# Optimization experiments

Measured on AMD Instinct MI355X. Metric: run time of the kernel, lower is better.

## Reference

```python
import jax, jax.numpy as jnp
import numpy as np
import math

EPS = 1e-5

def layernorm(x, w):
    mu = jnp.mean(x, axis=-1, keepdims=True)
    var = jnp.var(x, axis=-1, keepdims=True)
    return (x - mu) * jax.lax.rsqrt(var + EPS) * w

def setup_inputs() -> dict:
    key = jax.random.key(0)
    ks = jax.random.split(key, 6)
    B, T, C = 2, 2048, 768
    s = 0.02
    return {
        "x": jax.random.normal(ks[0], (B, T, C), jnp.float32),
        "w_ln1": jnp.ones((C,), jnp.float32),
        "w_attn": jax.random.normal(ks[1], (C, 3 * C), jnp.float32) * s,
        "w_attn_proj": jax.random.normal(ks[2], (C, C), jnp.float32) * s,
        "w_ln2": jnp.ones((C,), jnp.float32),
        "w_fc": jax.random.normal(ks[3], (C, 4 * C), jnp.float32) * s,
        "w_mlp_proj": jax.random.normal(ks[4], (4 * C, C), jnp.float32) * s,
    }

def _attention(x, w_attn, w_attn_proj, n_head):
    B, T, C = x.shape
    D = C // n_head
    qkv = x @ w_attn  # [B,T,3C]
    q, k, v = jnp.split(qkv, 3, axis=-1)
    # [B,H,T,D]
    q = q.reshape(B, T, n_head, D).transpose(0, 2, 1, 3)
    k = k.reshape(B, T, n_head, D).transpose(0, 2, 1, 3)
    v = v.reshape(B, T, n_head, D).transpose(0, 2, 1, 3)
    # squared L2 distance via ||q||^2 + ||k||^2 - 2 q.k (same math, no [B,H,T,T,D] tensor)
    q2 = jnp.sum(q * q, axis=-1)  # [B,H,T]
    k2 = jnp.sum(k * k, axis=-1)  # [B,H,T]
    qk = jnp.einsum('bhqd,bhkd->bhqk', q, k)
    sq_l2 = q2[..., :, None] + k2[..., None, :] - 2.0 * qk  # [B,H,T,T]
    scale = -1.0 / (2.0 * math.sqrt(D))
    scores = jnp.exp(sq_l2 * scale)
    causal = jnp.tril(jnp.ones((T, T), bool))
    scores = jnp.where(causal[None, None], scores, 0.0)
    y = jnp.einsum('bhqk,bhkd->bhqd', scores, v)
    y = y.transpose(0, 2, 1, 3).reshape(B, T, C)
    return y @ w_attn_proj

def reference(x, w_ln1, w_attn, w_attn_proj, w_ln2, w_fc, w_mlp_proj):
    n_head = 12
    x = x + _attention(layernorm(x, w_ln1), w_attn, w_attn_proj, n_head)
    h = layernorm(x, w_ln2)
    h = jax.nn.gelu(h @ w_fc, approximate=False) @ w_mlp_proj
    return x + h
```

## Files before the change

### kernel.cpp

```cpp
#include <hip/hip_runtime.h>

typedef unsigned short u16;
typedef unsigned int u32;
typedef short bf16x8 __attribute__((ext_vector_type(8)));
typedef float f32x4 __attribute__((ext_vector_type(4)));

#define AS1 __attribute__((address_space(1)))
#define AS3 __attribute__((address_space(3)))

#if __has_builtin(__builtin_amdgcn_exp2f)
#define EX2(x) __builtin_amdgcn_exp2f(x)
#else
#define EX2(x) exp2f(x)
#endif

__device__ __forceinline__ float bf2f(u16 u){ return __uint_as_float(((u32)u)<<16); }
__device__ __forceinline__ u16 f2bf(float f){
  u32 x = __float_as_uint(f);
  x += 0x7fffu + ((x>>16)&1u);
  return (u16)(x>>16);
}
__device__ __forceinline__ float gelu_exact(float x){
  return 0.5f*x*(1.f + erff(x*0.7071067811865475f));
}

__global__ __launch_bounds__(256) void transpose_cast(
    const float* __restrict__ w, u16* __restrict__ wt, int K, int N)
{
  __shared__ float t[32][33];
  int lx = threadIdx.x & 31, ly = threadIdx.x >> 5;
  int n0 = blockIdx.x*32, k0 = blockIdx.y*32;
  #pragma unroll
  for (int j=0;j<4;j++) t[ly+j*8][lx] = w[(long)(k0+ly+j*8)*N + n0+lx];
  __syncthreads();
  #pragma unroll
  for (int j=0;j<4;j++) wt[(long)(n0+ly+j*8)*K + k0+lx] = f2bf(t[lx][ly+j*8]);
}

__global__ __launch_bounds__(256) void ln_rows(
    const float* __restrict__ x, const float* __restrict__ w, u16* __restrict__ out)
{
  int row = blockIdx.x, tid = threadIdx.x;
  const float* xr = x + (long)row*768;
  float v0 = xr[tid], v1 = xr[tid+256], v2 = xr[tid+512];
  float s = v0+v1+v2, sq = v0*v0+v1*v1+v2*v2;
  #pragma unroll
  for (int o=32;o>=1;o>>=1){ s += __shfl_down(s,o); sq += __shfl_down(sq,o); }
  __shared__ float red[8];
  int wv = tid>>6, ln = tid&63;
  if (ln==0){ red[wv]=s; red[wv+4]=sq; }
  __syncthreads();
  float S  = red[0]+red[1]+red[2]+red[3];
  float SQ = red[4]+red[5]+red[6]+red[7];
  float mu = S*(1.f/768.f);
  float var = SQ*(1.f/768.f) - mu*mu;
  float rstd = rsqrtf(var + 1e-5f);
  u16* o = out + (long)row*768;
  o[tid]     = f2bf((v0-mu)*rstd*w[tid]);
  o[tid+256] = f2bf((v1-mu)*rstd*w[tid+256]);
  o[tid+512] = f2bf((v2-mu)*rstd*w[tid+512]);
}

__global__ __launch_bounds__(256) void reduce2_ln(
    const float* __restrict__ p, const float* __restrict__ resid,
    const float* __restrict__ w, float* __restrict__ x2, u16* __restrict__ xln, long n)
{
  int row = blockIdx.x, tid = threadIdx.x;
  long off = (long)row*768;
  float v[3];
  #pragma unroll
  for (int j=0;j<3;j++){
    long i = off + tid + j*256;
    v[j] = resid[i] + p[i] + p[n+i];
    x2[i] = v[j];
  }
  float s = v[0]+v[1]+v[2], sq = v[0]*v[0]+v[1]*v[1]+v[2]*v[2];
  #pragma unroll
  for (int o=32;o>=1;o>>=1){ s += __shfl_down(s,o); sq += __shfl_down(sq,o); }
  __shared__ float red[8];
  int wv = tid>>6, ln = tid&63;
  if (ln==0){ red[wv]=s; red[wv+4]=sq; }
  __syncthreads();
  float S  = red[0]+red[1]+red[2]+red[3];
  float SQ = red[4]+red[5]+red[6]+red[7];
  float mu = S*(1.f/768.f);
  float var = SQ*(1.f/768.f) - mu*mu;
  float rstd = rsqrtf(var + 1e-5f);
  #pragma unroll
  for (int j=0;j<3;j++)
    xln[off + tid + j*256] = f2bf((v[j]-mu)*rstd*w[tid + j*256]);
}

__global__ __launch_bounds__(256) void v_transpose(
    const u16* __restrict__ qkv, u16* __restrict__ vt)
{
  __shared__ __align__(16) u16 t[64*72];
  int b = blockIdx.z, h = blockIdx.y, t0 = blockIdx.x*64;
  int tid = threadIdx.x;
  int r = tid>>2, g = tid&3, c8 = g*16;
  const u16* src = qkv + ((long)(b*2048 + t0 + r))*2304 + 1536 + h*64 + c8;
  int wcol = c8 ^ (((r>>4)&3)*16);
  *(uint4*)&t[r*72 + wcol]     = *(const uint4*)src;
  *(uint4*)&t[r*72 + wcol + 8] = *(const uint4*)(src + 8);
  __syncthreads();
  int d = r;
  int rcol = d ^ (g*16);
  u32 pk[8];
  #pragma unroll
  for (int j=0;j<8;j++){
    u32 lo = t[(c8+2*j  )*72 + rcol];
    u32 hi = t[(c8+2*j+1)*72 + rcol];
    pk[j] = lo | (hi<<16);
  }
  u16* dst = vt + ((long)((b*12+h)*64 + d))*2048 + t0 + c8;
  uint4 o0 = {pk[0],pk[1],pk[2],pk[3]};
  uint4 o1 = {pk[4],pk[5],pk[6],pk[7]};
  *(uint4*)dst       = o0;
  *(uint4*)(dst + 8) = o1;
}

template<int EPI>
__global__ __launch_bounds__(256) void gemm_bt(
    const u16* __restrict__ A, const u16* __restrict__ BT,
    int M, int N, int K,
    u16* __restrict__ outB,
    float* __restrict__ q2g, float* __restrict__ k2g)
{
  __shared__ __align__(16) u16 As[2][128*32];
  __shared__ __align__(16) u16 Bs[2][128*32];
  int tid = threadIdx.x;
  int gx = gridDim.x;
  int nwg = gx * gridDim.y;
  int flat = blockIdx.x + gx*blockIdx.y;
  int cpx = nwg >> 3;
  int swz = (flat & 7)*cpx + (flat >> 3);
  int n0 = (swz % gx)*128, m0 = (swz / gx)*128;
  int w = tid>>6, lane = tid&63, lr = lane&15, lg = lane>>4;
  int wr = w>>1, wc = w&1;
  f32x4 acc[4][4];
  f32x4 z = {0.f,0.f,0.f,0.f};
  #pragma unroll
  for (int m=0;m<4;m++)
    #pragma unroll
    for (int n=0;n<4;n++) acc[m][n] = z;
  int rr16 = lane>>2, cc = (lane&3)*8;
  const u16* gA0 = A  + (long)(m0 + (2*w  )*16 + rr16)*K + cc;
  const u16* gA1 = A  + (long)(m0 + (2*w+1)*16 + rr16)*K + cc;
  const u16* gB0 = BT + (long)(n0 + (2*w  )*16 + rr16)*K + cc;
  const u16* gB1 = BT + (long)(n0 + (2*w+1)*16 + rr16)*K + cc;
  int o0 = (2*w)*512, o1 = (2*w+1)*512;
  __builtin_amdgcn_global_load_lds((const AS1 void*)gA0, (AS3 void*)(&As[0][o0]), 16, 0, 0);
  __builtin_amdgcn_global_load_lds((const AS1 void*)gA1, (AS3 void*)(&As[0][o1]), 16, 0, 0);
  __builtin_amdgcn_global_load_lds((const AS1 void*)gB0, (AS3 void*)(&Bs[0][o0]), 16, 0, 0);
  __builtin_amdgcn_global_load_lds((const AS1 void*)gB1, (AS3 void*)(&Bs[0][o1]), 16, 0, 0);
  gA0 += 32; gA1 += 32; gB0 += 32; gB1 += 32;
  int cur = 0;
  for (int k0=0; k0<K; k0+=32){
    __builtin_amdgcn_s_barrier();
    if (k0+32 < K){
      int nx = cur^1;
      __builtin_amdgcn_global_load_lds((const AS1 void*)gA0, (AS3 void*)(&As[nx][o0]), 16, 0, 0);
      __builtin_amdgcn_global_load_lds((const AS1 void*)gA1, (AS3 void*)(&As[nx][o1]), 16, 0, 0);
      __builtin_amdgcn_global_load_lds((const AS1 void*)gB0, (AS3 void*)(&Bs[nx][o0]), 16, 0, 0);
      __builtin_amdgcn_global_load_lds((const AS1 void*)gB1, (AS3 void*)(&Bs[nx][o1]), 16, 0, 0);
      gA0 += 32; gA1 += 32; gB0 += 32; gB1 += 32;
      asm volatile("s_waitcnt vmcnt(4)" ::: "memory");
    } else {
      asm volatile("s_waitcnt vmcnt(0)" ::: "memory");
    }
    __builtin_amdgcn_sched_barrier(0);
    const u16* Ac = As[cur];
    const u16* Bc = Bs[cur];
    bf16x8 af[4], bfr[4];
    #pragma unroll
    for (int m=0;m<4;m++) af[m]  = *(const bf16x8*)&Ac[(wr*64+m*16+lr)*32 + lg*8];
    #pragma unroll
    for (int n=0;n<4;n++) bfr[n] = *(const bf16x8*)&Bc[(wc*64+n*16+lr)*32 + lg*8];
    #pragma unroll
    for (int m=0;m<4;m++)
      #pragma unroll
      for (int n=0;n<4;n++)
        acc[m][n] = __builtin_amdgcn_mfma_f32_16x16x32_bf16(af[m], bfr[n], acc[m][n], 0,0,0);
    cur ^= 1;
  }
  if (EPI==0){
    #pragma unroll
    for (int m=0;m<4;m++){
      float s2[4] = {0.f,0.f,0.f,0.f};
      #pragma unroll
      for (int n=0;n<4;n++)
        #pragma unroll
        for (int r=0;r<4;r++){
          int row = m0 + wr*64 + m*16 + lg*4 + r;
          int col = n0 + wc*64 + n*16 + lr;
          u16 ub = f2bf(acc[m][n][r]);
          outB[(long)row*N + col] = ub;
          float vr = bf2f(ub);
          s2[r] += vr*vr;
        }
      #pragma unroll
      for (int r=0;r<4;r++){
        float t = s2[r];
        t += __shfl_xor(t,1); t += __shfl_xor(t,2); t += __shfl_xor(t,4); t += __shfl_xor(t,8);
        if (lr==0){
          int head = (n0 + wc*64) >> 6;
          int row = m0 + wr*64 + m*16 + lg*4 + r;
          int bb = row >> 11, tt = row & 2047;
          if (head < 12)      q2g[((long)(bb*12 + head     ))*2048 + tt] = t;
          else if (head < 24) k2g[((long)(bb*12 + head - 12))*2048 + tt] = t;
        }
      }
    }
  } else {
    #pragma unroll
    for (int m=0;m<4;m++)
      #pragma unroll
      for (int n=0;n<4;n++)
        #pragma unroll
        for (int r=0;r<4;r++){
          int row = m0 + wr*64 + m*16 + lg*4 + r;
          int col = n0 + wc*64 + n*16 + lr;
          outB[(long)row*N + col] = f2bf(gelu_exact(acc[m][n][r]));
        }
  }
}

__global__ __launch_bounds__(256) void gemm_ks(
    const u16* __restrict__ A, const u16* __restrict__ BT,
    int M, int N, int K, int KS,
    float* __restrict__ pb)
{
  __shared__ __align__(16) u16 As[2][128*32];
  __shared__ __align__(16) u16 Bs[2][64*32];
  int tid = threadIdx.x;
  int n0 = blockIdx.x*64, m0 = blockIdx.y*128;
  int kbeg = blockIdx.z*KS;
  int w = tid>>6, lane = tid&63, lr = lane&15, lg = lane>>4;
  int wr = w>>1, wc = w&1;
  f32x4 acc[4][2];
  f32x4 z = {0.f,0.f,0.f,0.f};
  #pragma unroll
  for (int m=0;m<4;m++){ acc[m][0]=z; acc[m][1]=z; }
  int rr16 = lane>>2, cc = (lane&3)*8;
  const u16* gA0 = A  + (long)(m0 + (2*w  )*16 + rr16)*K + kbeg + cc;
  const u16* gA1 = A  + (long)(m0 + (2*w+1)*16 + rr16)*K + kbeg + cc;
  const u16* gB0 = BT + (long)(n0 + w*16 + rr16)*K + kbeg + cc;
  int oa0 = (2*w)*512, oa1 = (2*w+1)*512, ob = w*512;
  __builtin_amdgcn_global_load_lds((const AS1 void*)gA0, (AS3 void*)(&As[0][oa0]), 16, 0, 0);
  __builtin_amdgcn_global_load_lds((const AS1 void*)gA1, (AS3 void*)(&As[0][oa1]), 16, 0, 0);
  __builtin_amdgcn_global_load_lds((const AS1 void*)gB0, (AS3 void*)(&Bs[0][ob ]), 16, 0, 0);
  gA0 += 32; gA1 += 32; gB0 += 32;
  int cur = 0;
  for (int k0=0; k0<KS; k0+=32){
    __builtin_amdgcn_s_barrier();
    if (k0+32 < KS){
      int nx = cur^1;
      __builtin_amdgcn_global_load_lds((const AS1 void*)gA0, (AS3 void*)(&As[nx][oa0]), 16, 0, 0);
      __builtin_amdgcn_global_load_lds((const AS1 void*)gA1, (AS3 void*)(&As[nx][oa1]), 16, 0, 0);
      __builtin_amdgcn_global_load_lds((const AS1 void*)gB0, (AS3 void*)(&Bs[nx][ob ]), 16, 0, 0);
      gA0 += 32; gA1 += 32; gB0 += 32;
      asm volatile("s_waitcnt vmcnt(3)" ::: "memory");
    } else {
      asm volatile("s_waitcnt vmcnt(0)" ::: "memory");
    }
    __builtin_amdgcn_sched_barrier(0);
    const u16* Ac = As[cur];
    const u16* Bc = Bs[cur];
    bf16x8 af[4], bfr[2];
    #pragma unroll
    for (int m=0;m<4;m++) af[m]  = *(const bf16x8*)&Ac[(wr*64+m*16+lr)*32 + lg*8];
    #pragma unroll
    for (int n=0;n<2;n++) bfr[n] = *(const bf16x8*)&Bc[(wc*32+n*16+lr)*32 + lg*8];
    #pragma unroll
    for (int m=0;m<4;m++)
      #pragma unroll
      for (int n=0;n<2;n++)
        acc[m][n] = __builtin_amdgcn_mfma_f32_16x16x32_bf16(af[m], bfr[n], acc[m][n], 0,0,0);
    cur ^= 1;
  }
  long zofs = (long)blockIdx.z*M*N;
  #pragma unroll
  for (int m=0;m<4;m++)
    #pragma unroll
    for (int n=0;n<2;n++)
      #pragma unroll
      for (int r=0;r<4;r++){
        int row = m0 + wr*64 + m*16 + lg*4 + r;
        int col = n0 + wc*32 + n*16 + lr;
        pb[zofs + (long)row*N + col] = acc[m][n][r];
      }
}

__global__ __launch_bounds__(256) void reduce2(
    const float* __restrict__ p, const float* __restrict__ resid,
    float* __restrict__ out, long n)
{
  long i = ((long)blockIdx.x*256 + threadIdx.x)*4;
  f32x4 a = *(const f32x4*)(resid+i);
  f32x4 b = *(const f32x4*)(p+i);
  f32x4 c = *(const f32x4*)(p+n+i);
  *(f32x4*)(out+i) = a+b+c;
}

__global__ __launch_bounds__(128) void attn_fused(
    const u16* __restrict__ qkv, const u16* __restrict__ vt,
    const float* __restrict__ q2g, const float* __restrict__ k2g,
    u16* __restrict__ Y)
{
  constexpr int C3=2304, C=768, T=2048, PADP=72;
  constexpr float C1 = 0.18033688f;
  constexpr float S2 = 0.09016844f;
  __shared__ __align__(16) u16 Ks[2][4096];
  __shared__ __align__(16) u16 Vs[2][4096];
  __shared__ __align__(16) u16 Ps[2][16*PADP];
  int bz = blockIdx.x;
  int swzb = (bz&7)*96 + (bz>>3);
  int sp = swzb & 31;
  int hh = (swzb>>5) % 12;
  int b  = swzb / 384;
  int tid = threadIdx.x, w = tid>>6, lane = tid&63, lr = lane&15, lg = lane>>4;
  long base = (long)b*T;
  long bh = (long)(b*12 + hh);
  const u16* kbase = qkv + base*C3 + C + hh*64;
  const u16* vbase = vt + bh*64*(long)T;
  const float* k2p = k2g + bh*T;
  const float* q2p0 = q2g + bh*T;

  int rowl = lane>>3;
  int c16 = (lane&7) ^ rowl;
  const u16* kp[4]; const u16* vp[4];
  #pragma unroll
  for (int i=0;i<4;i++){
    int c = w*4 + i;
    kp[i] = kbase + (long)(c*8 + rowl)*C3 + c16*8;
    vp[i] = vbase + (long)(c*8 + rowl)*T + c16*8;
  }
  u16* Pw = &Ps[w][0];
  f32x4 z = {0.f,0.f,0.f,0.f};

  for (int ph=0; ph<2; ++ph){
    int s = ph ? 63 - sp : sp;
    int ktl = s>>1;
    int qg0 = s*32 + w*16;
    const u16* qrow = qkv + (base + qg0 + lr)*C3 + hh*64;
    bf16x8 aq0 = *(const bf16x8*)(qrow + lg*8);
    bf16x8 aq1 = *(const bf16x8*)(qrow + 32 + lg*8);
    const float q2v = S2 * q2p0[qg0 + lr];
    const int qg_s = qg0 + lr;
    f32x4 accY[4];
    #pragma unroll
    for (int i=0;i<4;i++) accY[i] = z;

    #pragma unroll
    for (int i=0;i<4;i++){
      __builtin_amdgcn_global_load_lds((const AS1 void*)kp[i], (AS3 void*)&Ks[0][(w*4+i)*512], 16, 0, 0);
      __builtin_amdgcn_global_load_lds((const AS1 void*)vp[i], (AS3 void*)&Vs[0][(w*4+i)*512], 16, 0, 0);
    }
    f32x4 k2n4[4];
    #pragma unroll
    for (int nf=0;nf<4;nf++){
      f32x4 t4 = *(const f32x4*)&k2p[nf*16 + lg*4];
      k2n4[nf] = t4 * S2;
    }
    __syncthreads();

    int cur = 0;
    for (int kt=0; kt<=ktl; ++kt){
      f32x4 k2c4[4];
      #pragma unroll
      for (int i=0;i<4;i++) k2c4[i] = k2n4[i];
      if (kt < ktl){
        long kadd = (long)(kt+1)*64*C3;
        long vadd = (long)(kt+1)*64;
        #pragma unroll
        for (int i=0;i<4;i++){
          __builtin_amdgcn_global_load_lds((const AS1 void*)(kp[i]+kadd), (AS3 void*)&Ks[cur^1][(w*4+i)*512], 16, 0, 0);
          __builtin_amdgcn_global_load_lds((const AS1 void*)(vp[i]+vadd), (AS3 void*)&Vs[cur^1][(w*4+i)*512], 16, 0, 0);
        }
        #pragma unroll
        for (int nf=0;nf<4;nf++){
          f32x4 t4 = *(const f32x4*)&k2p[(kt+1)*64 + nf*16 + lg*4];
          k2n4[nf] = t4 * S2;
        }
      }
      const u16* Kc = &Ks[cur][0];
      const u16* Vc = &Vs[cur][0];
      int kg0 = kt*64;
      #pragma unroll
      for (int nf=0;nf<4;nf++){
        int row = nf*16 + lr;
        int sw0 = ((lg    ) ^ (row&7))*8;
        int sw1 = ((4 | lg) ^ (row&7))*8;
        bf16x8 kb0 = *(const bf16x8*)&Kc[row*64 + sw0];
        bf16x8 kb1 = *(const bf16x8*)&Kc[row*64 + sw1];
        f32x4 sc = z;
        sc = __builtin_amdgcn_mfma_f32_16x16x32_bf16(kb0, aq0, sc, 0,0,0);
        sc = __builtin_amdgcn_mfma_f32_16x16x32_bf16(kb1, aq1, sc, 0,0,0);
        int kb = kg0 + nf*16 + lg*4;
        u16 pbk[4];
        #pragma unroll
        for (int rr=0;rr<4;rr++){
          float arg = sc[rr]*C1 - q2v - k2c4[nf][rr];
          float e = EX2(arg);
          e = (kb + rr <= qg_s) ? e : 0.f;
          pbk[rr] = f2bf(e);
        }
        uint2 pk2;
        pk2.x = (u32)pbk[0] | ((u32)pbk[1]<<16);
        pk2.y = (u32)pbk[2] | ((u32)pbk[3]<<16);
        *(uint2*)&Pw[lr*PADP + nf*16 + lg*4] = pk2;
      }
      __builtin_amdgcn_wave_barrier();
      asm volatile("s_waitcnt lgkmcnt(0)" ::: "memory");
      bf16x8 ap0 = *(const bf16x8*)&Pw[lr*PADP + lg*8];
      bf16x8 ap1 = *(const bf16x8*)&Pw[lr*PADP + 32 + lg*8];
      #pragma unroll
      for (int nf=0;nf<4;nf++){
        int row = nf*16 + lr;
        int sw0 = ((lg    ) ^ (row&7))*8;
        int sw1 = ((4 | lg) ^ (row&7))*8;
        accY[nf] = __builtin_amdgcn_mfma_f32_16x16x32_bf16(ap0, *(const bf16x8*)&Vc[row*64 + sw0], accY[nf], 0,0,0);
        accY[nf] = __builtin_amdgcn_mfma_f32_16x16x32_bf16(ap1, *(const bf16x8*)&Vc[row*64 + sw1], accY[nf], 0,0,0);
      }
      __syncthreads();
      cur ^= 1;
    }
    #pragma unroll
    for (int nf=0;nf<4;nf++)
      #pragma unroll
      for (int rr=0;rr<4;rr++)
        Y[(base + qg0 + lg*4 + rr)*C + hh*64 + nf*16 + lr] = f2bf(accY[nf][rr]);
  }
}

extern "C" void kernel_launch(void* const* d_in, const int* in_sizes, int n_in,
                              void* d_out, int out_size, void* d_ws, size_t ws_size,
                              hipStream_t stream)
{
  (void)in_sizes; (void)n_in; (void)out_size; (void)ws_size;
  const float* x      = (const float*)d_in[0];
  const float* w_ln1  = (const float*)d_in[1];
  const float* w_attn = (const float*)d_in[2];
  const float* w_ap   = (const float*)d_in[3];
  const float* w_ln2  = (const float*)d_in[4];
  const float* w_fc   = (const float*)d_in[5];
  const float* w_mlp  = (const float*)d_in[6];
  float* out = (float*)d_out;
  const int M = 4096, T = 2048;
  const long NROW = (long)M*768;

  u16* ws      = (u16*)d_ws;
  u16* wT_attn = ws;
  u16* wT_ap   = wT_attn + 2304*768;
  u16* wT_fc   = wT_ap   + 768*768;
  u16* wT_mlp  = wT_fc   + 3072*768;
  u16* xln     = wT_mlp  + 768*3072;
  u16* qkvb    = xln     + 4096*768;
  u16* Ybuf    = qkvb    + 4096*2304;
  u16* hbuf    = qkvb;
  float* x2    = (float*)(Ybuf + 4096*768);
  u16* vtb     = (u16*)(x2 + 4096*768);
  float* q2g   = (float*)(vtb + 2*12*64*2048);
  float* k2g   = q2g + 24*2048;
  float* pbuf  = k2g + 24*2048;

  dim3 blk(256);
  transpose_cast<<<dim3(2304/32,  768/32), blk, 0, stream>>>(w_attn, wT_attn,  768, 2304);
  transpose_cast<<<dim3( 768/32,  768/32), blk, 0, stream>>>(w_ap,   wT_ap,    768,  768);
  transpose_cast<<<dim3(3072/32,  768/32), blk, 0, stream>>>(w_fc,   wT_fc,    768, 3072);
  transpose_cast<<<dim3( 768/32, 3072/32), blk, 0, stream>>>(w_mlp,  wT_mlp,  3072,  768);

  ln_rows<<<dim3(M), blk, 0, stream>>>(x, w_ln1, xln);
  gemm_bt<0><<<dim3(2304/128, M/128), blk, 0, stream>>>(xln, wT_attn, M, 2304, 768, qkvb, q2g, k2g);
  v_transpose<<<dim3(T/64, 12, 2), blk, 0, stream>>>(qkvb, vtb);
  attn_fused<<<dim3(2*12*32), dim3(128), 0, stream>>>(qkvb, vtb, q2g, k2g, Ybuf);
  gemm_ks<<<dim3(768/64, M/128, 2), blk, 0, stream>>>(Ybuf, wT_ap, M, 768, 768, 384, pbuf);
  reduce2_ln<<<dim3(M), blk, 0, stream>>>(pbuf, x, w_ln2, x2, xln, NROW);
  gemm_bt<1><<<dim3(3072/128, M/128), blk, 0, stream>>>(xln, wT_fc, M, 3072, 768, hbuf, nullptr, nullptr);
  gemm_ks<<<dim3(768/64, M/128, 2), blk, 0, stream>>>(hbuf, wT_mlp, M, 768, 3072, 1536, pbuf);
  reduce2<<<dim3(NROW/1024), blk, 0, stream>>>(pbuf, x2, out, NROW);
}
```

Before: 291.5 us.

## Split attention into one query tile per block and load V directly to registers

```diff
diff --git a/kernel.cpp b/kernel.cpp
--- a/kernel.cpp
+++ b/kernel.cpp
@@ -311,13 +311,12 @@
   constexpr float C1 = 0.18033688f;
   constexpr float S2 = 0.09016844f;
   __shared__ __align__(16) u16 Ks[2][4096];
-  __shared__ __align__(16) u16 Vs[2][4096];
   __shared__ __align__(16) u16 Ps[2][16*PADP];
   int bz = blockIdx.x;
-  int swzb = (bz&7)*96 + (bz>>3);
-  int sp = swzb & 31;
-  int hh = (swzb>>5) % 12;
-  int b  = swzb / 384;
+  int swzb = (bz&7)*192 + (bz>>3);
+  int s  = 63 - (swzb & 63);
+  int hh = (swzb>>6) % 12;
+  int b  = swzb / 768;
   int tid = threadIdx.x, w = tid>>6, lane = tid&63, lr = lane&15, lg = lane>>4;
   long base = (long)b*T;
   long bh = (long)(b*12 + hh);
@@ -328,109 +327,103 @@
 
   int rowl = lane>>3;
   int c16 = (lane&7) ^ rowl;
-  const u16* kp[4]; const u16* vp[4];
+  const u16* kp[4];
   #pragma unroll
   for (int i=0;i<4;i++){
     int c = w*4 + i;
     kp[i] = kbase + (long)(c*8 + rowl)*C3 + c16*8;
-    vp[i] = vbase + (long)(c*8 + rowl)*T + c16*8;
   }
   u16* Pw = &Ps[w][0];
   f32x4 z = {0.f,0.f,0.f,0.f};
 
-  for (int ph=0; ph<2; ++ph){
-    int s = ph ? 63 - sp : sp;
-    int ktl = s>>1;
-    int qg0 = s*32 + w*16;
-    const u16* qrow = qkv + (base + qg0 + lr)*C3 + hh*64;
-    bf16x8 aq0 = *(const bf16x8*)(qrow + lg*8);
-    bf16x8 aq1 = *(const bf16x8*)(qrow + 32 + lg*8);
-    const float q2v = S2 * q2p0[qg0 + lr];
-    const int qg_s = qg0 + lr;
-    f32x4 accY[4];
-    #pragma unroll
-    for (int i=0;i<4;i++) accY[i] = z;
-
-    #pragma unroll
-    for (int i=0;i<4;i++){
-      __builtin_amdgcn_global_load_lds((const AS1 void*)kp[i], (AS3 void*)&Ks[0][(w*4+i)*512], 16, 0, 0);
-      __builtin_amdgcn_global_load_lds((const AS1 void*)vp[i], (AS3 void*)&Vs[0][(w*4+i)*512], 16, 0, 0);
-    }
-    f32x4 k2n4[4];
+  int ktl = s>>1;
+  int qg0 = s*32 + w*16;
+  const u16* qrow = qkv + (base + qg0 + lr)*C3 + hh*64;
+  bf16x8 aq0 = *(const bf16x8*)(qrow + lg*8);
+  bf16x8 aq1 = *(const bf16x8*)(qrow + 32 + lg*8);
+  const float q2v = S2 * q2p0[qg0 + lr];
+  const int qg_s = qg0 + lr;
+  f32x4 accY[4];
+  #pragma unroll
+  for (int i=0;i<4;i++) accY[i] = z;
+
+  #pragma unroll
+  for (int i=0;i<4;i++)
+    __builtin_amdgcn_global_load_lds((const AS1 void*)kp[i], (AS3 void*)&Ks[0][(w*4+i)*512], 16, 0, 0);
+  f32x4 k2n4[4];
+  #pragma unroll
+  for (int nf=0;nf<4;nf++){
+    f32x4 t4 = *(const f32x4*)&k2p[nf*16 + lg*4];
+    k2n4[nf] = t4 * S2;
+  }
+  __syncthreads();
+
+  int cur = 0;
+  for (int kt=0; kt<=ktl; ++kt){
+    int kg0 = kt*64;
+    f32x4 k2c4[4];
+    #pragma unroll
+    for (int i=0;i<4;i++) k2c4[i] = k2n4[i];
+    uint4 vr[8];
     #pragma unroll
     for (int nf=0;nf<4;nf++){
-      f32x4 t4 = *(const f32x4*)&k2p[nf*16 + lg*4];
-      k2n4[nf] = t4 * S2;
+      const u16* vpn = vbase + (long)(nf*16 + lr)*T + kg0 + lg*8;
+      vr[2*nf  ] = *(const uint4*)(vpn);
+      vr[2*nf+1] = *(const uint4*)(vpn + 32);
+    }
+    if (kt < ktl){
+      long kadd = (long)(kt+1)*64*C3;
+      #pragma unroll
+      for (int i=0;i<4;i++)
+        __builtin_amdgcn_global_load_lds((const AS1 void*)(kp[i]+kadd), (AS3 void*)&Ks[cur^1][(w*4+i)*512], 16, 0, 0);
+      #pragma unroll
+      for (int nf=0;nf<4;nf++){
+        f32x4 t4 = *(const f32x4*)&k2p[(kt+1)*64 + nf*16 + lg*4];
+        k2n4[nf] = t4 * S2;
+      }
+    }
+    const u16* Kc = &Ks[cur][0];
+    #pragma unroll
+    for (int nf=0;nf<4;nf++){
+      int row = nf*16 + lr;
+      int sw0 = ((lg    ) ^ (row&7))*8;
+      int sw1 = ((4 | lg) ^ (row&7))*8;
+      bf16x8 kb0 = *(const bf16x8*)&Kc[row*64 + sw0];
+      bf16x8 kb1 = *(const bf16x8*)&Kc[row*64 + sw1];
+      f32x4 sc = z;
+      sc = __builtin_amdgcn_mfma_f32_16x16x32_bf16(kb0, aq0, sc, 0,0,0);
+      sc = __builtin_amdgcn_mfma_f32_16x16x32_bf16(kb1, aq1, sc, 0,0,0);
+      int kb = kg0 + nf*16 + lg*4;
+      u16 pbk[4];
+      #pragma unroll
+      for (int rr=0;rr<4;rr++){
+        float arg = sc[rr]*C1 - q2v - k2c4[nf][rr];
+        float e = EX2(arg);
+        e = (kb + rr <= qg_s) ? e : 0.f;
+        pbk[rr] = f2bf(e);
+      }
+      uint2 pk2;
+      pk2.x = (u32)pbk[0] | ((u32)pbk[1]<<16);
+      pk2.y = (u32)pbk[2] | ((u32)pbk[3]<<16);
+      *(uint2*)&Pw[lr*PADP + nf*16 + lg*4] = pk2;
+    }
+    __builtin_amdgcn_wave_barrier();
+    asm volatile("s_waitcnt lgkmcnt(0)" ::: "memory");
+    bf16x8 ap0 = *(const bf16x8*)&Pw[lr*PADP + lg*8];
+    bf16x8 ap1 = *(const bf16x8*)&Pw[lr*PADP + 32 + lg*8];
+    #pragma unroll
+    for (int nf=0;nf<4;nf++){
+      accY[nf] = __builtin_amdgcn_mfma_f32_16x16x32_bf16(ap0, *(const bf16x8*)&vr[2*nf  ], accY[nf], 0,0,0);
+      accY[nf] = __builtin_amdgcn_mfma_f32_16x16x32_bf16(ap1, *(const bf16x8*)&vr[2*nf+1], accY[nf], 0,0,0);
     }
     __syncthreads();
-
-    int cur = 0;
-    for (int kt=0; kt<=ktl; ++kt){
-      f32x4 k2c4[4];
-      #pragma unroll
-      for (int i=0;i<4;i++) k2c4[i] = k2n4[i];
-      if (kt < ktl){
-        long kadd = (long)(kt+1)*64*C3;
-        long vadd = (long)(kt+1)*64;
-        #pragma unroll
-        for (int i=0;i<4;i++){
-          __builtin_amdgcn_global_load_lds((const AS1 void*)(kp[i]+kadd), (AS3 void*)&Ks[cur^1][(w*4+i)*512], 16, 0, 0);
-          __builtin_amdgcn_global_load_lds((const AS1 void*)(vp[i]+vadd), (AS3 void*)&Vs[cur^1][(w*4+i)*512], 16, 0, 0);
-        }
-        #pragma unroll
-        for (int nf=0;nf<4;nf++){
-          f32x4 t4 = *(const f32x4*)&k2p[(kt+1)*64 + nf*16 + lg*4];
-          k2n4[nf] = t4 * S2;
-        }
-      }
-      const u16* Kc = &Ks[cur][0];
-      const u16* Vc = &Vs[cur][0];
-      int kg0 = kt*64;
-      #pragma unroll
-      for (int nf=0;nf<4;nf++){
-        int row = nf*16 + lr;
-        int sw0 = ((lg    ) ^ (row&7))*8;
-        int sw1 = ((4 | lg) ^ (row&7))*8;
-        bf16x8 kb0 = *(const bf16x8*)&Kc[row*64 + sw0];
-        bf16x8 kb1 = *(const bf16x8*)&Kc[row*64 + sw1];
-        f32x4 sc = z;
-        sc = __builtin_amdgcn_mfma_f32_16x16x32_bf16(kb0, aq0, sc, 0,0,0);
-        sc = __builtin_amdgcn_mfma_f32_16x16x32_bf16(kb1, aq1, sc, 0,0,0);
-        int kb = kg0 + nf*16 + lg*4;
-        u16 pbk[4];
-        #pragma unroll
-        for (int rr=0;rr<4;rr++){
-          float arg = sc[rr]*C1 - q2v - k2c4[nf][rr];
-          float e = EX2(arg);
-          e = (kb + rr <= qg_s) ? e : 0.f;
-          pbk[rr] = f2bf(e);
-        }
-        uint2 pk2;
-        pk2.x = (u32)pbk[0] | ((u32)pbk[1]<<16);
-        pk2.y = (u32)pbk[2] | ((u32)pbk[3]<<16);
-        *(uint2*)&Pw[lr*PADP + nf*16 + lg*4] = pk2;
-      }
-      __builtin_amdgcn_wave_barrier();
-      asm volatile("s_waitcnt lgkmcnt(0)" ::: "memory");
-      bf16x8 ap0 = *(const bf16x8*)&Pw[lr*PADP + lg*8];
-      bf16x8 ap1 = *(const bf16x8*)&Pw[lr*PADP + 32 + lg*8];
-      #pragma unroll
-      for (int nf=0;nf<4;nf++){
-        int row = nf*16 + lr;
-        int sw0 = ((lg    ) ^ (row&7))*8;
-        int sw1 = ((4 | lg) ^ (row&7))*8;
-        accY[nf] = __builtin_amdgcn_mfma_f32_16x16x32_bf16(ap0, *(const bf16x8*)&Vc[row*64 + sw0], accY[nf], 0,0,0);
-        accY[nf] = __builtin_amdgcn_mfma_f32_16x16x32_bf16(ap1, *(const bf16x8*)&Vc[row*64 + sw1], accY[nf], 0,0,0);
-      }
-      __syncthreads();
-      cur ^= 1;
-    }
-    #pragma unroll
-    for (int nf=0;nf<4;nf++)
-      #pragma unroll
-      for (int rr=0;rr<4;rr++)
-        Y[(base + qg0 + lg*4 + rr)*C + hh*64 + nf*16 + lr] = f2bf(accY[nf][rr]);
-  }
+    cur ^= 1;
+  }
+  #pragma unroll
+  for (int nf=0;nf<4;nf++)
+    #pragma unroll
+    for (int rr=0;rr<4;rr++)
+      Y[(base + qg0 + lg*4 + rr)*C + hh*64 + nf*16 + lr] = f2bf(accY[nf][rr]);
 }
 
 extern "C" void kernel_launch(void* const* d_in, const int* in_sizes, int n_in,
@@ -473,7 +466,7 @@
   ln_rows<<<dim3(M), blk, 0, stream>>>(x, w_ln1, xln);
   gemm_bt<0><<<dim3(2304/128, M/128), blk, 0, stream>>>(xln, wT_attn, M, 2304, 768, qkvb, q2g, k2g);
   v_transpose<<<dim3(T/64, 12, 2), blk, 0, stream>>>(qkvb, vtb);
-  attn_fused<<<dim3(2*12*32), dim3(128), 0, stream>>>(qkvb, vtb, q2g, k2g, Ybuf);
+  attn_fused<<<dim3(2*12*64), dim3(128), 0, stream>>>(qkvb, vtb, q2g, k2g, Ybuf);
   gemm_ks<<<dim3(768/64, M/128, 2), blk, 0, stream>>>(Ybuf, wT_ap, M, 768, 768, 384, pbuf);
   reduce2_ln<<<dim3(M), blk, 0, stream>>>(pbuf, x, w_ln2, x2, xln, NROW);
   gemm_bt<1><<<dim3(3072/128, M/128), blk, 0, stream>>>(xln, wT_fc, M, 3072, 768, hbuf, nullptr, nullptr);
```

Measured after the change: 326.1 us. 1.12x slower.
